# Kernel tuning notes

Measured on AMD Instinct MI355X. Metric: run time of the kernel, lower is better.

Reference implementation:

```python
import jax, jax.numpy as jnp
import numpy as np

N_NODES = 16384
K_NBR = 16
N_HOPS = 4  # hops + 2
IN_DIM = 256
RAW_DIM = 128
OUT_DIM = 64
PHI_DIM = 16
N_KERN = 4
E = N_NODES * K_NBR


def setup_inputs() -> dict:
    key = jax.random.key(0)
    ks = jax.random.split(key, 16)
    s = 0.05  # small weight scale for numerical sanity
    h = jax.random.normal(ks[0], (N_NODES, IN_DIM), jnp.float32)
    e_tensor = jax.random.normal(ks[1], (N_HOPS, N_NODES, RAW_DIM), jnp.float32)
    # kNN-style edges: each dst node has exactly K_NBR incoming edges
    src = jax.random.randint(ks[2], (N_HOPS, E), 0, N_NODES, jnp.int32)
    dst = jnp.tile(jnp.repeat(jnp.arange(N_NODES, dtype=jnp.int32), K_NBR)[None, :], (N_HOPS, 1))
    return {
        'h': h,
        'e_tensor': e_tensor,
        'src': src,
        'dst': dst,
        'W_phi': jax.random.normal(ks[3], (N_HOPS, RAW_DIM, PHI_DIM - 1), jnp.float32) * s,
        'mlp_w1': jax.random.normal(ks[4], (N_HOPS, RAW_DIM, IN_DIM), jnp.float32) * s,
        'mlp_b1': jax.random.normal(ks[5], (N_HOPS, IN_DIM), jnp.float32) * s,
        'mlp_w2': jax.random.normal(ks[6], (N_HOPS, IN_DIM, PHI_DIM * N_KERN), jnp.float32) * s,
        'mlp_b2': jax.random.normal(ks[7], (N_HOPS, PHI_DIM * N_KERN), jnp.float32) * s,
        'tilde_phi': jax.random.normal(ks[8], (N_HOPS, N_KERN, PHI_DIM), jnp.float32),
        'W': jax.random.normal(ks[9], (N_HOPS, IN_DIM, OUT_DIM * N_KERN), jnp.float32) * s,
        'bias': jax.random.normal(ks[10], (N_HOPS, OUT_DIM), jnp.float32) * s,
        'z': jax.random.normal(ks[11], (OUT_DIM, 1), jnp.float32),
    }


def _deform_gconv(h, e_l, src, dst, W_phi, w1, b1, w2, b2, tilde_phi, W, bias):
    N = h.shape[0]
    nk, phi_dim = tilde_phi.shape
    hk = (h @ W).reshape(N, nk, -1)                                  # (N, nk, out)
    phi = e_l @ W_phi                                                # (N, phi-1)
    tn = tilde_phi / jnp.linalg.norm(tilde_phi, axis=1, keepdims=True)  # (nk, phi)
    hid = jax.nn.relu(e_l @ w1 + b1)
    delta = (hid @ w2 + b2).reshape(N, nk, phi_dim)                  # (N, nk, phi)
    delta_ik = tn[None, :, :] + delta                                # (N, nk, phi)
    # per-edge quantities (edges carry dst-node delta_ik, u_sub_v distance)
    dist = phi[src] - phi[dst]                                       # (E, phi-1)
    last = jnp.all(dist == 0, axis=1, keepdims=True).astype(dist.dtype)
    dist = jnp.concatenate([dist, last], axis=1)                     # (E, phi)
    dist = dist / jnp.maximum(jnp.linalg.norm(dist, axis=1, keepdims=True), 1e-8)
    logits = jnp.einsum('ep,ekp->ek', dist, delta_ik[dst])           # (E, nk)
    # edge_softmax over incoming edges of each dst node
    mx = jax.ops.segment_max(logits, dst, num_segments=N)
    ex = jnp.exp(logits - mx[dst])
    den = jax.ops.segment_sum(ex, dst, num_segments=N)
    att = ex / den[dst]                                              # (E, nk)
    # message passing: m = h[src] * att, sum over incoming edges
    m = hk[src] * att[:, :, None]                                    # (E, nk, out)
    agg = jax.ops.segment_sum(m, dst, num_segments=N)                # (N, nk, out)
    out = agg.sum(1) + bias[None, :]
    out = out / jnp.maximum(jnp.linalg.norm(out, axis=1, keepdims=True), 1e-8)
    # regularizers
    d = tn[:, None, :] - tn[None, :, :]                              # (nk, nk, phi)
    l_sep = jnp.sum(jnp.sum(d * d, axis=-1)) / nk                    # sum_i mean_j ||t_i - t_j||^2
    l_focus = jnp.mean(jnp.sum(delta * delta, axis=2))
    return out, l_sep, l_focus


def reference(h, e_tensor, src, dst, W_phi, mlp_w1, mlp_b1, mlp_w2, mlp_b2, tilde_phi, W, bias, z):
    outs, l_seps, l_fos = jax.vmap(
        _deform_gconv, in_axes=(None, 0, 0, 0, 0, 0, 0, 0, 0, 0, 0, 0)
    )(h, e_tensor, src, dst, W_phi, mlp_w1, mlp_b1, mlp_w2, mlp_b2, tilde_phi, W, bias)
    # hop-level softmax fusion
    score = jnp.einsum('hno,oz->hnz', outs, z)                       # (n_hops, N, 1)
    att = jax.nn.softmax(score, axis=0)
    tilde_h = jnp.sum(att * outs, axis=0)                            # (N, out)
    l_sep = jnp.mean(l_seps)
    l_focus = jnp.mean(l_fos)
    return tilde_h, l_sep, l_focus
```

## Files before the change

### kernel.cpp

```cpp
#include <hip/hip_runtime.h>
#include <hip/hip_bf16.h>

#define N_NODES 16384
#define K_NBR 16
#define HOPS 4
#define IN_DIM 256
#define RAW_DIM 128
#define OUT_DIM 64
#define PHI_DIM 16
#define N_KERN 4
#define E_EDGES (N_NODES * K_NBR)

typedef __hip_bfloat16 bf16;
typedef __attribute__((ext_vector_type(8))) short short8;
typedef __attribute__((ext_vector_type(4))) float f32x4;
typedef __attribute__((ext_vector_type(2))) float f32x2;
typedef __attribute__((ext_vector_type(4))) unsigned int uint4v;

__device__ __forceinline__ float toF(float x) { return x; }
__device__ __forceinline__ float toF(bf16 x) { return __bfloat162float(x); }
__device__ __forceinline__ short f2bfbits(float f)
{
    bf16 b = __float2bfloat16(f);
    short s; __builtin_memcpy(&s, &b, 2); return s;
}

#define SWZ(row, colShort) ((colShort) ^ (((row) & 7) << 3))

__device__ __forceinline__ void gld_lds16(const bf16* g, short* l)
{
    __builtin_amdgcn_global_load_lds(
        (const __attribute__((address_space(1))) unsigned int*)g,
        (__attribute__((address_space(3))) unsigned int*)l, 16, 0, 0);
}

template <int IMM>
__device__ __forceinline__ float swzx(float v)
{
    return __builtin_bit_cast(float,
        __builtin_amdgcn_ds_swizzle(__builtin_bit_cast(int, v), IMM));
}
#define XOR1  0x041F
#define XOR2  0x081F
#define XOR4  0x101F
#define XOR8  0x201F
#define XOR16 0x401F

__device__ __forceinline__ void pkfma_w0(f32x2& acc, f32x2 w, f32x2 x)
{
    asm("v_pk_fma_f32 %0, %1, %2, %0 op_sel:[0,0,0] op_sel_hi:[0,1,1]"
        : "+v"(acc) : "v"(w), "v"(x));
}
__device__ __forceinline__ void pkfma_w1(f32x2& acc, f32x2 w, f32x2 x)
{
    asm("v_pk_fma_f32 %0, %1, %2, %0 op_sel:[1,0,0] op_sel_hi:[1,1,1]"
        : "+v"(acc) : "v"(w), "v"(x));
}

#define CVC_B1   0
#define CVC_B2   (CVC_B1 + HOPS * IN_DIM)
#define CVC_BIAS (CVC_B2 + HOPS * PHI_DIM * N_KERN)
#define CVC_Z    (CVC_BIAS + HOPS * OUT_DIM)
#define CVC_END  (CVC_Z + OUT_DIM)

#define WT_N  (HOPS * 256 * 256)
#define W1T_N (HOPS * 256 * 128)
#define W2T_N (HOPS * 64 * 256)
#define WPT_N (HOPS * 16 * 128)
#define CVT_TOTAL (WT_N + W1T_N + W2T_N + WPT_N)

#define NB_CV ((CVC_END + 255) / 256)
#define NB_WT (CVT_TOTAL / 1024)
#define NB_H  (N_NODES * 256 / 8 / 2048)
#define NB_E  (HOPS * N_NODES * 128 / 8 / 2048)
#define NB_ALL (NB_CV + NB_WT + NB_H + NB_E + 1)

#define GA_TOTAL 2048

__device__ __forceinline__ float loadDyn(const void* p, int i, bool isbf)
{
    return isbf ? toF(((const bf16*)p)[i]) : ((const float*)p)[i];
}

__device__ __forceinline__ void cvt8(bf16* dst, const void* src, size_t base, bool isbf)
{
    short8 v;
    if (isbf) {
        v = *(const short8*)((const bf16*)src + base);
    } else {
        const float* sp = (const float*)src + base;
        f32x4 f0 = *(const f32x4*)sp;
        f32x4 f1 = *(const f32x4*)(sp + 4);
#pragma unroll
        for (int j = 0; j < 4; j++) { v[j] = f2bfbits(f0[j]); v[4 + j] = f2bfbits(f1[j]); }
    }
    *(short8*)(dst + base) = v;
}

__global__ __launch_bounds__(256) void cvt_all(
    const void* h, const void* e,
    const void* wphi, const void* w1, const void* b1, const void* w2,
    const void* b2, const void* tphi, const void* W, const void* bias,
    const void* z, float* __restrict__ CV,
    bf16* __restrict__ wt, bf16* __restrict__ w1t, bf16* __restrict__ w2t,
    bf16* __restrict__ wpt, bf16* __restrict__ h_bf, bf16* __restrict__ e_bf,
    float* __restrict__ tn_out, float* __restrict__ acc, int* __restrict__ flagOut)
{
    __shared__ float s_det[4];
    int tid = threadIdx.x;
    {
        unsigned short pv = ((const unsigned short*)h)[tid];
        unsigned int bits = ((unsigned int)pv) << 16;
        float v; __builtin_memcpy(&v, &bits, 4);
        v = fabsf(v);
        if (!(v == v) || v > 1e30f) v = 1e30f;
#pragma unroll
        for (int off = 32; off > 0; off >>= 1) v = fmaxf(v, __shfl_xor(v, off));
        if ((tid & 63) == 0) s_det[tid >> 6] = v;
    }
    __syncthreads();
    bool isbf = fmaxf(fmaxf(s_det[0], s_det[1]), fmaxf(s_det[2], s_det[3])) < 1e4f;

    int b = blockIdx.x;
    if (b == NB_ALL - 1) {
        __shared__ float s_v[256], s_tn[256], s_red[256], s_hop[4];
        int hop = tid >> 6, t64 = tid & 63;
        int row = t64 >> 4, p = t64 & 15;
        float v = loadDyn(tphi, hop * 64 + t64, isbf);
        s_v[tid] = v;
        __syncthreads();
        float ss = 0.f;
        for (int q = 0; q < 16; q++) { float x = s_v[hop * 64 + row * 16 + q]; ss += x * x; }
        float tnv = v / sqrtf(ss);
        tn_out[hop * 64 + t64] = tnv;
        s_tn[tid] = tnv;
        __syncthreads();
        float s = 0.f;
        for (int j = 0; j < 4; j++) {
            float d = tnv - s_tn[hop * 64 + j * 16 + p];
            s += d * d;
        }
        s_red[tid] = s;
        __syncthreads();
        if (t64 == 0) {
            float tot = 0.f;
            for (int i = 0; i < 64; i++) tot += s_red[hop * 64 + i];
            s_hop[hop] = tot;
        }
        __syncthreads();
        if (tid == 0) {
            acc[0] = (s_hop[0] + s_hop[1] + s_hop[2] + s_hop[3]) * 0.0625f;
            acc[1] = 0.f;
            *flagOut = isbf ? 1 : 0;
        }
        return;
    }
    if (b < NB_CV) {
        int idx = b * 256 + tid;
        if (idx >= CVC_END) return;
        float v;
        if      (idx < CVC_B2)   v = loadDyn(b1,   idx - CVC_B1,   isbf);
        else if (idx < CVC_BIAS) v = loadDyn(b2,   idx - CVC_B2,   isbf);
        else if (idx < CVC_Z)    v = loadDyn(bias, idx - CVC_BIAS, isbf);
        else                     v = loadDyn(z,    idx - CVC_Z,    isbf);
        CV[idx] = v;
        return;
    }
    b -= NB_CV;
    if (b < NB_WT) {
        int base = (b * 256 + tid) * 4;
#pragma unroll
        for (int jj = 0; jj < 4; jj++) {
            int idx = base + jj;
            if (idx < WT_N) {
                int o = idx, hop = o >> 16, rem = o & 65535, n = rem >> 8, k = rem & 255;
                wt[o] = __float2bfloat16(loadDyn(W, hop * 65536 + k * 256 + n, isbf));
            } else if (idx < WT_N + W1T_N) {
                int o = idx - WT_N, hop = o >> 15, rem = o & 32767, n = rem >> 7, k = rem & 127;
                w1t[o] = __float2bfloat16(loadDyn(w1, hop * 32768 + k * 256 + n, isbf));
            } else if (idx < WT_N + W1T_N + W2T_N) {
                int o = idx - WT_N - W1T_N, hop = o >> 14, rem = o & 16383, n = rem >> 8, k = rem & 255;
                w2t[o] = __float2bfloat16(loadDyn(w2, hop * 16384 + k * 64 + n, isbf));
            } else {
                int o = idx - WT_N - W1T_N - W2T_N, hop = o >> 11, rem = o & 2047, n = rem >> 7, k = rem & 127;
                float v = (n < 15) ? loadDyn(wphi, hop * 1920 + k * 15 + n, isbf) : 0.f;
                wpt[o] = __float2bfloat16(v);
            }
        }
        return;
    }
    b -= NB_WT;
    if (b < NB_H) {
#pragma unroll
        for (int k = 0; k < 8; k++) {
            size_t base = ((size_t)b * 2048 + k * 256 + tid) * 8;
            cvt8(h_bf, h, base, isbf);
        }
        return;
    }
    b -= NB_H;
    {
#pragma unroll
        for (int k = 0; k < 8; k++) {
            size_t base = ((size_t)b * 2048 + k * 256 + tid) * 8;
            cvt8(e_bf, e, base, isbf);
        }
    }
}

__device__ __forceinline__ void gemm_hk_dev(
    char* smem, const bf16* __restrict__ A, const bf16* __restrict__ Bt,
    unsigned char* __restrict__ Cg, int colBase, int rowBase)
{
    short* base = (short*)smem;
    int tid = threadIdx.x;
    int w = tid >> 6, lane = tid & 63;
    int wr = w >> 1, wc = w & 1;
    int l16 = lane & 15, quad = lane >> 4;
    f32x4 acc[4][4] = {};

#define HK_STAGE(bufb, k0v)                                                          \
    {                                                                                \
        short* As_ = base + (bufb) * 16384;                                          \
        short* Bs_ = As_ + 8192;                                                     \
        for (int id = tid; id < 128 * 8; id += 256) {                                \
            int row = id >> 3, j = id & 7;                                           \
            gld_lds16(A + (size_t)(rowBase + row) * 256 + (k0v) + ((j ^ (row & 7)) * 8), \
                      As_ + id * 8);                                                 \
        }                                                                            \
        for (int id = tid; id < 128 * 8; id += 256) {                                \
            int row = id >> 3, j = id & 7;                                           \
            gld_lds16(Bt + (size_t)(colBase + row) * 256 + (k0v) + ((j ^ (row & 7)) * 8), \
                      Bs_ + id * 8);                                                 \
        }                                                                            \
    }

    HK_STAGE(0, 0)
    HK_STAGE(1, 64)
    asm volatile("s_waitcnt vmcnt(8)" ::: "memory");
    __builtin_amdgcn_sched_barrier(0);
    __builtin_amdgcn_s_barrier();
    __builtin_amdgcn_sched_barrier(0);
#pragma unroll
    for (int t = 0; t < 4; ++t) {
        short* As = base + (t & 1) * 16384;
        short* Bs = As + 8192;
        short8 aF[2][4], bF[2][4];
#pragma unroll
        for (int hh = 0; hh < 2; hh++) {
            int kc = hh * 32;
#pragma unroll
            for (int mi = 0; mi < 4; mi++) {
                int row = wr * 64 + mi * 16 + l16;
                aF[hh][mi] = *(const short8*)&As[row * 64 + SWZ(row, kc + quad * 8)];
            }
#pragma unroll
            for (int ni = 0; ni < 4; ni++) {
                int row = wc * 64 + ni * 16 + l16;
                bF[hh][ni] = *(const short8*)&Bs[row * 64 + SWZ(row, kc + quad * 8)];
            }
        }
        asm volatile("s_waitcnt lgkmcnt(0)" ::: "memory");
        __builtin_amdgcn_sched_barrier(0);
        __builtin_amdgcn_s_barrier();
        __builtin_amdgcn_sched_barrier(0);
        if (t < 2) HK_STAGE(t & 1, (t + 2) * 64)
#pragma unroll
        for (int hh = 0; hh < 2; hh++)
#pragma unroll
            for (int mi = 0; mi < 4; mi++)
#pragma unroll
                for (int ni = 0; ni < 4; ni++)
                    acc[mi][ni] = __builtin_amdgcn_mfma_f32_16x16x32_bf16(
                        aF[hh][mi], bF[hh][ni], acc[mi][ni], 0, 0, 0);
        if (t < 3) {
            if (t < 2) { asm volatile("s_waitcnt vmcnt(8)" ::: "memory"); }
            else       { asm volatile("s_waitcnt vmcnt(0)" ::: "memory"); }
            __builtin_amdgcn_sched_barrier(0);
            __builtin_amdgcn_s_barrier();
            __builtin_amdgcn_sched_barrier(0);
        }
    }
#undef HK_STAGE

    unsigned char* Cs = (unsigned char*)smem;
#pragma unroll
    for (int mi = 0; mi < 4; mi++)
#pragma unroll
        for (int ni = 0; ni < 4; ni++) {
            int cl = wc * 64 + ni * 16 + l16;
#pragma unroll
            for (int r = 0; r < 4; r++) {
                int rl = wr * 64 + mi * 16 + quad * 4 + r;
                float v = acc[mi][ni][r];
                int pk = __builtin_amdgcn_cvt_pk_fp8_f32(v, v, 0, false);
                Cs[rl * 128 + cl] = (unsigned char)(pk & 0xFF);
            }
        }
    __syncthreads();
    for (int c = tid; c < 128 * 8; c += 256) {
        int r = c >> 3, off = (c & 7) * 16;
        *(uint4v*)(Cg + ((size_t)(rowBase + r) * 256 + colBase) + off) =
            *(const uint4v*)(Cs + (size_t)r * 128 + off);
    }
}

__device__ __forceinline__ void hid_delta_dev(
    char* smem,
    const bf16* __restrict__ A, const bf16* __restrict__ B1,
    const bf16* __restrict__ B2, const bf16* __restrict__ WP,
    const float* __restrict__ b1, const float* __restrict__ b2,
    const float* __restrict__ tn, float* __restrict__ Dg,
    float* __restrict__ phiG, float* __restrict__ lfocus, int rowBase)
{
    short* As  = (short*)smem;
    short* Bs  = As + 4096;
    short* Wpa = As + 20480;
    short* Hs  = (short*)smem;
    short* B2s = Hs + 16384;
    float* Ds  = (float*)smem;
    float* s_w = (float*)(smem + 65520);

    int tid = threadIdx.x;
    int w = tid >> 6, lane = tid & 63;
    int l16 = lane & 15, quad = lane >> 4;

    {
        f32x4 acc[4][4] = {};
        f32x4 accp[4] = {};
        for (int k0 = 0; k0 < 128; k0 += 64) {
            for (int id = tid; id < 64 * 8; id += 256) {
                int row = id >> 3, j = id & 7;
                gld_lds16(A + (size_t)(rowBase + row) * 128 + k0 + ((j ^ (row & 7)) * 8),
                          As + id * 8);
            }
            for (int id = tid; id < 256 * 8; id += 256) {
                int row = id >> 3, j = id & 7;
                gld_lds16(B1 + (size_t)row * 128 + k0 + ((j ^ (row & 7)) * 8),
                          Bs + id * 8);
            }
            if (k0 == 0) {
                int row = tid >> 4, j = tid & 15;
                gld_lds16(WP + (size_t)row * 128 + ((j ^ (row & 7)) * 8),
                          Wpa + tid * 8);
            }
            __syncthreads();
#pragma unroll
            for (int kc = 0; kc < 64; kc += 32) {
                short8 aF[4], bF[4];
#pragma unroll
                for (int mi = 0; mi < 4; mi++) {
                    int row = mi * 16 + l16;
                    aF[mi] = *(const short8*)&As[row * 64 + SWZ(row, kc + quad * 8)];
                }
#pragma unroll
                for (int ni = 0; ni < 4; ni++) {
                    int row = w * 64 + ni * 16 + l16;
                    bF[ni] = *(const short8*)&Bs[row * 64 + SWZ(row, kc + quad * 8)];
                }
#pragma unroll
                for (int mi = 0; mi < 4; mi++)
#pragma unroll
                    for (int ni = 0; ni < 4; ni++)
                        acc[mi][ni] = __builtin_amdgcn_mfma_f32_16x16x32_bf16(
                            aF[mi], bF[ni], acc[mi][ni], 0, 0, 0);
                if (w == 0) {
                    short8 bFp = *(const short8*)&Wpa[l16 * 128 + SWZ(l16, k0 + kc + quad * 8)];
#pragma unroll
                    for (int mi = 0; mi < 4; mi++)
                        accp[mi] = __builtin_amdgcn_mfma_f32_16x16x32_bf16(
                            aF[mi], bFp, accp[mi], 0, 0, 0);
                }
            }
            __syncthreads();
        }
#pragma unroll
        for (int mi = 0; mi < 4; mi++) {
#pragma unroll
            for (int ni = 0; ni < 4; ni++) {
                int col = w * 64 + ni * 16 + l16;
                float bv = b1[col];
#pragma unroll
                for (int r = 0; r < 4; r++) {
                    int row = mi * 16 + quad * 4 + r;
                    float v = fmaxf(acc[mi][ni][r] + bv, 0.f);
                    Hs[row * 256 + SWZ(row, col)] = f2bfbits(v);
                }
            }
        }
        for (int id = tid; id < 64 * 32; id += 256) {
            int row = id >> 5, j = id & 31;
            gld_lds16(B2 + (size_t)row * 256 + ((j ^ (row & 7)) * 8),
                      B2s + id * 8);
        }
        if (w == 0) {
#pragma unroll
            for (int mi = 0; mi < 4; mi++)
#pragma unroll
                for (int r = 0; r < 4; r++)
                    phiG[(size_t)(rowBase + mi * 16 + quad * 4 + r) * 16 + l16] =
                        accp[mi][r];
        }
    }

    {
        __syncthreads();
        f32x4 acc2[4] = {};
        int arow = w * 16 + l16;
#pragma unroll
        for (int q = 0; q < 8; q++) {
            int kc = q * 32;
            short8 aF = *(const short8*)&Hs[arow * 256 + SWZ(arow, kc + quad * 8)];
            short8 bFq[4];
#pragma unroll
            for (int ni = 0; ni < 4; ni++) {
                int brow = ni * 16 + l16;
                bFq[ni] = *(const short8*)&B2s[brow * 256 + SWZ(brow, kc + quad * 8)];
            }
#pragma unroll
            for (int ni = 0; ni < 4; ni++)
                acc2[ni] = __builtin_amdgcn_mfma_f32_16x16x32_bf16(aF, bFq[ni], acc2[ni], 0, 0, 0);
        }
        asm volatile("s_waitcnt lgkmcnt(0)" ::: "memory");
        __builtin_amdgcn_sched_barrier(0);
        __builtin_amdgcn_s_barrier();
        __builtin_amdgcn_sched_barrier(0);
        float sq = 0.f;
#pragma unroll
        for (int ni = 0; ni < 4; ni++) {
            int col = ni * 16 + l16;
            float bv = b2[col], tv = tn[col];
#pragma unroll
            for (int r = 0; r < 4; r++) {
                int row = w * 16 + quad * 4 + r;
                float v = acc2[ni][r] + bv;
                sq += v * v;
                Ds[row * 64 + col] = v + tv;
            }
        }
#pragma unroll
        for (int off = 32; off > 0; off >>= 1) sq += __shfl_xor(sq, off);
        if (lane == 0) s_w[w] = sq;
        __syncthreads();
        for (int c = tid; c < 64 * 16; c += 256) {
            int r = c >> 4, off = (c & 15) * 4;
            *(uint4v*)(Dg + (size_t)(rowBase + r) * 64 + off) =
                *(const uint4v*)(Ds + (size_t)r * 64 + off);
        }
        if (tid == 0) atomicAdd(lfocus, s_w[0] + s_w[1] + s_w[2] + s_w[3]);
    }
}

__global__ __launch_bounds__(256, 2) void gemm_all(
    const bf16* __restrict__ h_bf, const bf16* __restrict__ e_bf,
    const bf16* __restrict__ WT, const bf16* __restrict__ WPT,
    const bf16* __restrict__ W1T, const bf16* __restrict__ W2T,
    const float* __restrict__ b1All, const float* __restrict__ b2All,
    const float* __restrict__ tnAll, unsigned char* __restrict__ hk_f8,
    float* __restrict__ phi, float* __restrict__ DELTA, float* __restrict__ lfocus)
{
    __shared__ __align__(16) char smem[65536];
    int b = blockIdx.x;
    int x = b & 7;
    int p = b >> 3;
    int s = p >> 1;
    if ((p & 1) == 0) {
        int rg = x * 16 + (s >> 3);
        int v = s & 7;
        int hop = v >> 1, part = v & 1;
        gemm_hk_dev(smem, h_bf, WT + (size_t)hop * 65536,
                    hk_f8 + (size_t)hop * N_NODES * 256, part * 128, rg * 128);
    } else {
        int hop = x & 3;
        int tile = ((x >> 2) << 7) + s;
        hid_delta_dev(smem,
            e_bf + (size_t)hop * N_NODES * 128,
            W1T + (size_t)hop * 32768, W2T + (size_t)hop * 16384,
            WPT + (size_t)hop * 2048,
            b1All + hop * 256, b2All + hop * 64, tnAll + hop * 64,
            DELTA + (size_t)hop * N_NODES * 64,
            phi + (size_t)hop * N_NODES * 16, lfocus, tile * 64);
    }
}

__global__ __launch_bounds__(256) void edge_agg2(
    const unsigned char* __restrict__ hk, const float* __restrict__ phi,
    const float* __restrict__ dik, const int* __restrict__ src,
    const float* __restrict__ biasAll, float* __restrict__ outs)
{
    int b = blockIdx.x;
    int hop = b & 3;
    int wave = threadIdx.x >> 6, lane = threadIdx.x & 63;
    int node = (b >> 2) * 4 + wave;
    const unsigned char* hk_l = hk + (size_t)hop * N_NODES * 256;
    const float* phi_l  = phi + (size_t)hop * N_NODES * 16;
    const float* dik_l  = dik + (size_t)hop * N_NODES * 64;
    const int*   src_n  = src + (size_t)hop * E_EDGES + (size_t)node * 16;
    const float* bias_l = biasAll + hop * 64;
    float*       outs_n = outs + ((size_t)hop * N_NODES + node) * 64;

    __shared__ __align__(16) float s_dik[4][64];
    __shared__ __align__(16) float s_attT[4][4][24];
    __shared__ int   s_src[4][16];

    s_dik[wave][lane] = dik_l[(size_t)node * 64 + lane];
    if (lane < 16) s_src[wave][lane] = src_n[lane];

    int e = lane >> 2, q = lane & 3;
    int sN = s_src[wave][e];
    f32x4 ps = *(const f32x4*)(phi_l + (size_t)sN * 16 + q * 4);
    f32x4 pd = *(const f32x4*)(phi_l + (size_t)node * 16 + q * 4);
    float d0 = ps[0] - pd[0], d1 = ps[1] - pd[1];
    float d2 = ps[2] - pd[2], d3 = ps[3] - pd[3];
    bool q3 = (q == 3);
    float ssp = d0 * d0 + d1 * d1 + d2 * d2 + (q3 ? 0.f : d3 * d3);
    ssp += swzx<XOR1>(ssp); ssp += swzx<XOR2>(ssp);
    float last = (ssp == 0.f) ? 1.f : 0.f;
    if (q3) d3 = last;
    float inv = fminf(__builtin_amdgcn_rsqf(ssp + last * last), 1e8f);
#pragma unroll
    for (int k = 0; k < 4; k++) {
        f32x4 dkv = *(const f32x4*)&s_dik[wave][k * 16 + q * 4];
        float pk = d0 * dkv[0] + d1 * dkv[1] + d2 * dkv[2] + d3 * dkv[3];
        pk += swzx<XOR1>(pk); pk += swzx<XOR2>(pk);
        if (q == k) s_attT[wave][k][e] = pk * inv;
    }

    int k2 = lane & 3;
    float lgv = s_attT[wave][k2][e];
    float mx = lgv;
    mx = fmaxf(mx, swzx<XOR4>(mx));
    mx = fmaxf(mx, swzx<XOR8>(mx));
    mx = fmaxf(mx, swzx<XOR16>(mx));
    mx = fmaxf(mx, __shfl_xor(mx, 32));
    float ex = __expf(lgv - mx);
    float den = ex;
    den += swzx<XOR4>(den);
    den += swzx<XOR8>(den);
    den += swzx<XOR16>(den);
    den += __shfl_xor(den, 32);
    s_attT[wave][k2][e] = ex * __builtin_amdgcn_rcpf(den);

    int kk = lane >> 4, dsub = (lane & 15) * 4;
    f32x2 att2[8];
#pragma unroll
    for (int g = 0; g < 8; g++) att2[g] = *(const f32x2*)&s_attT[wave][kk][g * 2];
    f32x2 a01 = {0.f, 0.f}, a23 = {0.f, 0.f};
#pragma unroll
    for (int ep = 0; ep < 8; ep++) {
        int sm0 = __builtin_amdgcn_readfirstlane(s_src[wave][2 * ep]);
        int sm1 = __builtin_amdgcn_readfirstlane(s_src[wave][2 * ep + 1]);
        unsigned int u0 = *(const unsigned int*)(hk_l + (size_t)sm0 * 256 + lane * 4);
        unsigned int u1 = *(const unsigned int*)(hk_l + (size_t)sm1 * 256 + lane * 4);
        f32x2 w = att2[ep];
        pkfma_w0(a01, w, __builtin_amdgcn_cvt_pk_f32_fp8((int)u0, false));
        pkfma_w0(a23, w, __builtin_amdgcn_cvt_pk_f32_fp8((int)u0, true));
        pkfma_w1(a01, w, __builtin_amdgcn_cvt_pk_f32_fp8((int)u1, false));
        pkfma_w1(a23, w, __builtin_amdgcn_cvt_pk_f32_fp8((int)u1, true));
    }
    float a0 = a01[0], a1 = a01[1], a2 = a23[0], a3 = a23[1];
    a0 += swzx<XOR16>(a0); a0 += __shfl_xor(a0, 32);
    a1 += swzx<XOR16>(a1); a1 += __shfl_xor(a1, 32);
    a2 += swzx<XOR16>(a2); a2 += __shfl_xor(a2, 32);
    a3 += swzx<XOR16>(a3); a3 += __shfl_xor(a3, 32);
    f32x4 bv = *(const f32x4*)(bias_l + dsub);
    float o0 = a0 + bv[0];
    float o1 = a1 + bv[1];
    float o2 = a2 + bv[2];
    float o3 = a3 + bv[3];
    float ssq = o0 * o0 + o1 * o1 + o2 * o2 + o3 * o3;
    ssq += swzx<XOR1>(ssq);
    ssq += swzx<XOR2>(ssq);
    ssq += swzx<XOR4>(ssq);
    ssq += swzx<XOR8>(ssq);
    float inv2 = fminf(__builtin_amdgcn_rsqf(ssq), 1e8f);
    if (kk == 0) {
        f32x4 st;
        st[0] = o0 * inv2; st[1] = o1 * inv2; st[2] = o2 * inv2; st[3] = o3 * inv2;
        *(f32x4*)(outs_n + dsub) = st;
    }
}

__global__ __launch_bounds__(256) void fuse_kernel(
    const float* __restrict__ outs, const float* __restrict__ z,
    void* __restrict__ out, const int* __restrict__ flag,
    const float* __restrict__ acc)
{
    int tid = threadIdx.x;
    int node = blockIdx.x * 4 + (tid >> 6);
    int dd = tid & 63;
    float zv = z[dd];
    float o[4], sc[4];
#pragma unroll
    for (int h = 0; h < 4; h++) {
        o[h] = outs[((size_t)h * N_NODES + node) * 64 + dd];
        float v = o[h] * zv;
#pragma unroll
        for (int off = 32; off > 0; off >>= 1) v += __shfl_xor(v, off);
        sc[h] = v;
    }
    float mx = fmaxf(fmaxf(sc[0], sc[1]), fmaxf(sc[2], sc[3]));
    float e0 = __expf(sc[0] - mx), e1 = __expf(sc[1] - mx);
    float e2 = __expf(sc[2] - mx), e3 = __expf(sc[3] - mx);
    float den = e0 + e1 + e2 + e3;
    float t = (e0 * o[0] + e1 * o[1] + e2 * o[2] + e3 * o[3]) * __builtin_amdgcn_rcpf(den);
    size_t oi = (size_t)node * 64 + dd;
    bool isbf = (*flag != 0);
    if (isbf) ((bf16*)out)[oi] = __float2bfloat16(t);
    else      ((float*)out)[oi] = t;
    if (blockIdx.x == 0 && tid == 0) {
        float a = acc[0];
        float b = acc[1] / ((float)N_NODES * 4.f * 4.f);
        size_t base = (size_t)N_NODES * 64;
        if (isbf) {
            ((bf16*)out)[base]     = __float2bfloat16(a);
            ((bf16*)out)[base + 1] = __float2bfloat16(b);
        } else {
            ((float*)out)[base]     = a;
            ((float*)out)[base + 1] = b;
        }
    }
}

extern "C" void kernel_launch(void* const* d_in, const int* in_sizes, int n_in,
                              void* d_out, int out_size, void* d_ws, size_t ws_size,
                              hipStream_t stream)
{
    const void* h    = d_in[0];
    const void* e    = d_in[1];
    const int*  src  = (const int*)d_in[2];
    const void* Wphi = d_in[4];
    const void* w1   = d_in[5];
    const void* b1   = d_in[6];
    const void* w2   = d_in[7];
    const void* b2   = d_in[8];
    const void* tphi = d_in[9];
    const void* W    = d_in[10];
    const void* bias = d_in[11];
    const void* z    = d_in[12];

    float* ws    = (float*)d_ws;
    float* CV    = ws;
    float* OUTS  = CV + CVC_END;
    float* PHI   = OUTS + (size_t)4 * N_NODES * 64;
    float* DELTA = PHI + (size_t)4 * N_NODES * 16;
    float* TN    = DELTA + (size_t)4 * N_NODES * 64;
    float* ACC   = TN + 256;
    int*   FLAG  = (int*)(ACC + 2);
    bf16*  H_BF  = (bf16*)(ACC + 4);
    bf16*  E_BF  = H_BF + (size_t)N_NODES * 256;
    bf16*  WT    = E_BF + (size_t)HOPS * N_NODES * 128;
    bf16*  W1T   = WT + WT_N;
    bf16*  W2T   = W1T + W1T_N;
    bf16*  WPT   = W2T + W2T_N;
    unsigned char* HK_F8 = (unsigned char*)(WPT + WPT_N);

    cvt_all<<<NB_ALL, 256, 0, stream>>>(
        h, e, Wphi, w1, b1, w2, b2, tphi, W, bias, z, CV,
        WT, W1T, W2T, WPT, H_BF, E_BF, TN, ACC, FLAG);

    gemm_all<<<dim3(GA_TOTAL), 256, 0, stream>>>(
        H_BF, E_BF, WT, WPT, W1T, W2T,
        CV + CVC_B1, CV + CVC_B2, TN, HK_F8, PHI, DELTA, ACC + 1);

    edge_agg2<<<dim3(N_NODES), 256, 0, stream>>>(
        HK_F8, PHI, DELTA, src, CV + CVC_BIAS, OUTS);

    fuse_kernel<<<dim3(N_NODES / 4), 256, 0, stream>>>(
        OUTS, CV + CVC_Z, d_out, FLAG, ACC);
}
```

Before: 195.6 us.

## Double-buffer hid GEMM K-loop with async LDS loads and add nontemporal memory ops

Splits the first hidden-layer GEMM's K loop into four 32-wide stages with two LDS buffers. The next stage is prefetched via global_load_lds while MFMAs run on the current one, synchronised with explicit vmcnt/lgkmcnt waits and barriers, and a new swizzle suits the 32-column tiles. It also switches several streaming global loads and stores (conversion, dik/src reads, per-hop outs, final output) to nontemporal hints to reduce cache pollution. Hand-written waitcnt values are fragile if the number of issued loads changes.

```diff
diff --git a/kernel.cpp b/kernel.cpp
--- a/kernel.cpp
+++ b/kernel.cpp
@@ -26,6 +26,7 @@
 }
 
 #define SWZ(row, colShort) ((colShort) ^ (((row) & 7) << 3))
+#define SWZ32(row, colShort) ((colShort) ^ ((((row) >> 1) & 3) << 3))
 
 __device__ __forceinline__ void gld_lds16(const bf16* g, short* l)
 {
@@ -86,11 +87,11 @@
 {
     short8 v;
     if (isbf) {
-        v = *(const short8*)((const bf16*)src + base);
+        v = __builtin_nontemporal_load((const short8*)((const bf16*)src + base));
     } else {
         const float* sp = (const float*)src + base;
-        f32x4 f0 = *(const f32x4*)sp;
-        f32x4 f1 = *(const f32x4*)(sp + 4);
+        f32x4 f0 = __builtin_nontemporal_load((const f32x4*)sp);
+        f32x4 f1 = __builtin_nontemporal_load((const f32x4*)(sp + 4));
 #pragma unroll
         for (int j = 0; j < 4; j++) { v[j] = f2bfbits(f0[j]); v[4 + j] = f2bfbits(f1[j]); }
     }
@@ -313,10 +314,9 @@
     const float* __restrict__ tn, float* __restrict__ Dg,
     float* __restrict__ phiG, float* __restrict__ lfocus, int rowBase)
 {
-    short* As  = (short*)smem;
-    short* Bs  = As + 4096;
-    short* Wpa = As + 20480;
-    short* Hs  = (short*)smem;
+    short* base = (short*)smem;
+    short* Wpa = base + 20480;
+    short* Hs  = base;
     short* B2s = Hs + 16384;
     float* Ds  = (float*)smem;
     float* s_w = (float*)(smem + 65520);
@@ -325,55 +325,81 @@
     int w = tid >> 6, lane = tid & 63;
     int l16 = lane & 15, quad = lane >> 4;
 
+#define HID_STAGE(bufb, k0v)                                                   \
+    {                                                                          \
+        short* As_ = base + (bufb) * 2048;                                     \
+        short* Bs_ = base + 4096 + (bufb) * 8192;                              \
+        for (int id = tid; id < 64 * 4; id += 256) {                           \
+            int row = id >> 2, j = id & 3;                                     \
+            gld_lds16(A + (size_t)(rowBase + row) * 128 + (k0v) +              \
+                          ((j ^ ((row >> 1) & 3)) * 8),                        \
+                      As_ + id * 8);                                           \
+        }                                                                      \
+        for (int id = tid; id < 256 * 4; id += 256) {                          \
+            int row = id >> 2, j = id & 3;                                     \
+            gld_lds16(B1 + (size_t)row * 128 + (k0v) +                         \
+                          ((j ^ ((row >> 1) & 3)) * 8),                        \
+                      Bs_ + id * 8);                                           \
+        }                                                                      \
+    }
+
+    f32x4 acc[4][4] = {};
+    f32x4 accp[4] = {};
     {
-        f32x4 acc[4][4] = {};
-        f32x4 accp[4] = {};
-        for (int k0 = 0; k0 < 128; k0 += 64) {
-            for (int id = tid; id < 64 * 8; id += 256) {
-                int row = id >> 3, j = id & 7;
-                gld_lds16(A + (size_t)(rowBase + row) * 128 + k0 + ((j ^ (row & 7)) * 8),
-                          As + id * 8);
-            }
-            for (int id = tid; id < 256 * 8; id += 256) {
-                int row = id >> 3, j = id & 7;
-                gld_lds16(B1 + (size_t)row * 128 + k0 + ((j ^ (row & 7)) * 8),
-                          Bs + id * 8);
-            }
-            if (k0 == 0) {
-                int row = tid >> 4, j = tid & 15;
-                gld_lds16(WP + (size_t)row * 128 + ((j ^ (row & 7)) * 8),
-                          Wpa + tid * 8);
-            }
-            __syncthreads();
-#pragma unroll
-            for (int kc = 0; kc < 64; kc += 32) {
-                short8 aF[4], bF[4];
-#pragma unroll
-                for (int mi = 0; mi < 4; mi++) {
-                    int row = mi * 16 + l16;
-                    aF[mi] = *(const short8*)&As[row * 64 + SWZ(row, kc + quad * 8)];
-                }
-#pragma unroll
-                for (int ni = 0; ni < 4; ni++) {
-                    int row = w * 64 + ni * 16 + l16;
-                    bF[ni] = *(const short8*)&Bs[row * 64 + SWZ(row, kc + quad * 8)];
-                }
+        HID_STAGE(0, 0)
+        {
+            int row = tid >> 4, j = tid & 15;
+            gld_lds16(WP + (size_t)row * 128 + ((j ^ (row & 7)) * 8),
+                      Wpa + tid * 8);
+        }
+        HID_STAGE(1, 32)
+        asm volatile("s_waitcnt vmcnt(5)" ::: "memory");
+        __builtin_amdgcn_sched_barrier(0);
+        __builtin_amdgcn_s_barrier();
+        __builtin_amdgcn_sched_barrier(0);
+#pragma unroll
+        for (int t = 0; t < 4; ++t) {
+            short* As_ = base + (t & 1) * 2048;
+            short* Bs_ = base + 4096 + (t & 1) * 8192;
+            short8 aF[4], bF[4], bFp;
+#pragma unroll
+            for (int mi = 0; mi < 4; mi++) {
+                int row = mi * 16 + l16;
+                aF[mi] = *(const short8*)&As_[row * 32 + SWZ32(row, quad * 8)];
+            }
+#pragma unroll
+            for (int ni = 0; ni < 4; ni++) {
+                int row = w * 64 + ni * 16 + l16;
+                bF[ni] = *(const short8*)&Bs_[row * 32 + SWZ32(row, quad * 8)];
+            }
+            if (w == 0)
+                bFp = *(const short8*)&Wpa[l16 * 128 + SWZ(l16, t * 32 + quad * 8)];
+            asm volatile("s_waitcnt lgkmcnt(0)" ::: "memory");
+            __builtin_amdgcn_sched_barrier(0);
+            __builtin_amdgcn_s_barrier();
+            __builtin_amdgcn_sched_barrier(0);
+            if (t < 2) HID_STAGE(t & 1, (t + 2) * 32)
+#pragma unroll
+            for (int mi = 0; mi < 4; mi++)
+#pragma unroll
+                for (int ni = 0; ni < 4; ni++)
+                    acc[mi][ni] = __builtin_amdgcn_mfma_f32_16x16x32_bf16(
+                        aF[mi], bF[ni], acc[mi][ni], 0, 0, 0);
+            if (w == 0) {
 #pragma unroll
                 for (int mi = 0; mi < 4; mi++)
-#pragma unroll
-                    for (int ni = 0; ni < 4; ni++)
-                        acc[mi][ni] = __builtin_amdgcn_mfma_f32_16x16x32_bf16(
-                            aF[mi], bF[ni], acc[mi][ni], 0, 0, 0);
-                if (w == 0) {
-                    short8 bFp = *(const short8*)&Wpa[l16 * 128 + SWZ(l16, k0 + kc + quad * 8)];
-#pragma unroll
-                    for (int mi = 0; mi < 4; mi++)
-                        accp[mi] = __builtin_amdgcn_mfma_f32_16x16x32_bf16(
-                            aF[mi], bFp, accp[mi], 0, 0, 0);
-                }
-            }
-            __syncthreads();
-        }
+                    accp[mi] = __builtin_amdgcn_mfma_f32_16x16x32_bf16(
+                        aF[mi], bFp, accp[mi], 0, 0, 0);
+            }
+            if (t < 3) {
+                if (t < 2) { asm volatile("s_waitcnt vmcnt(5)" ::: "memory"); }
+                else       { asm volatile("s_waitcnt vmcnt(0)" ::: "memory"); }
+                __builtin_amdgcn_sched_barrier(0);
+                __builtin_amdgcn_s_barrier();
+                __builtin_amdgcn_sched_barrier(0);
+            }
+        }
+#undef HID_STAGE
 #pragma unroll
         for (int mi = 0; mi < 4; mi++) {
 #pragma unroll
@@ -503,8 +529,8 @@
     __shared__ __align__(16) float s_attT[4][4][24];
     __shared__ int   s_src[4][16];
 
-    s_dik[wave][lane] = dik_l[(size_t)node * 64 + lane];
-    if (lane < 16) s_src[wave][lane] = src_n[lane];
+    s_dik[wave][lane] = __builtin_nontemporal_load(&dik_l[(size_t)node * 64 + lane]);
+    if (lane < 16) s_src[wave][lane] = __builtin_nontemporal_load(&src_n[lane]);
 
     int e = lane >> 2, q = lane & 3;
     int sN = s_src[wave][e];
@@ -577,7 +603,7 @@
     if (kk == 0) {
         f32x4 st;
         st[0] = o0 * inv2; st[1] = o1 * inv2; st[2] = o2 * inv2; st[3] = o3 * inv2;
-        *(f32x4*)(outs_n + dsub) = st;
+        __builtin_nontemporal_store(st, (f32x4*)(outs_n + dsub));
     }
 }
 
@@ -593,7 +619,7 @@
     float o[4], sc[4];
 #pragma unroll
     for (int h = 0; h < 4; h++) {
-        o[h] = outs[((size_t)h * N_NODES + node) * 64 + dd];
+        o[h] = __builtin_nontemporal_load(&outs[((size_t)h * N_NODES + node) * 64 + dd]);
         float v = o[h] * zv;
 #pragma unroll
         for (int off = 32; off > 0; off >>= 1) v += __shfl_xor(v, off);
@@ -606,8 +632,8 @@
     float t = (e0 * o[0] + e1 * o[1] + e2 * o[2] + e3 * o[3]) * __builtin_amdgcn_rcpf(den);
     size_t oi = (size_t)node * 64 + dd;
     bool isbf = (*flag != 0);
-    if (isbf) ((bf16*)out)[oi] = __float2bfloat16(t);
-    else      ((float*)out)[oi] = t;
+    if (isbf) __builtin_nontemporal_store(f2bfbits(t), (short*)out + oi);
+    else      __builtin_nontemporal_store(t, (float*)out + oi);
     if (blockIdx.x == 0 && tid == 0) {
         float a = acc[0];
         float b = acc[1] / ((float)N_NODES * 4.f * 4.f);
```

Result: no change. 196.4 us, median of 2 (+0.4%).
